# Performance work log

Hardware: AMD Instinct MI355X
Metric: run time of the kernel (lower is better)

The kernel has to match this reference:

```python
import jax, jax.numpy as jnp
import numpy as np
import math

SUB_LEN = 5

def _row_mask(index, sub_len, win_len):
    # Faithful port of logsparseAttention.row_mask (numpy, built at trace time).
    log_l = math.ceil(math.log2(sub_len))
    mask = np.zeros(win_len, dtype=np.float32)
    if (win_len // sub_len) * 2 * log_l > index:
        mask[: index + 1] = 1.0
    else:
        while index >= 0:
            if index - log_l + 1 < 0:
                mask[:index] = 1.0
                break
            mask[index - log_l + 1 : index + 1] = 1.0
            for i in range(log_l):
                new_index = index - log_l + 1 - 2 ** i
                if index - new_index <= sub_len and new_index >= 0:
                    mask[new_index] = 1.0
            index -= sub_len
    return mask

def _log_mask(win_len, sub_len):
    m = np.stack([_row_mask(i, sub_len, win_len) for i in range(win_len)])
    return m[None, None]  # [1, 1, L, L]

def setup_inputs() -> dict:
    key = jax.random.key(0)
    kq, kk, kv = jax.random.split(key, 3)
    B, L, H, D = 4, 2048, 16, 64
    return {
        "queries": jax.random.normal(kq, (B, L, H, D), dtype=jnp.float32),
        "keys": jax.random.normal(kk, (B, L, H, D), dtype=jnp.float32),
        "values": jax.random.normal(kv, (B, L, H, D), dtype=jnp.float32),
        "attn_mask": jnp.zeros((1,), dtype=jnp.int32),  # unused by the module
    }

def reference(queries, keys, values, attn_mask):
    L = queries.shape[1]
    mask = jnp.asarray(_log_mask(L, SUB_LEN), dtype=queries.dtype)  # [1,1,L,L]
    q = jnp.swapaxes(queries, 1, 2)            # [B, H, L, D]
    k = jnp.transpose(keys, (0, 2, 3, 1))      # [B, H, D, L]
    v = jnp.swapaxes(values, 1, 2)             # [B, H, L, D]
    pre_att = jnp.matmul(q, k)                 # [B, H, L, L] (no scaling: scale=None)
    pre_att = pre_att * mask + (-1e9) * (1.0 - mask)
    att = jax.nn.softmax(pre_att, axis=-1)
    return jnp.matmul(att, v)                  # [B, H, L, D]
```

## Files before the change

kernel.cpp:

```cpp
#include <hip/hip_runtime.h>


typedef __attribute__((ext_vector_type(8))) short short8;
typedef __attribute__((ext_vector_type(4))) float floatx4;
typedef _Float16 half8 __attribute__((ext_vector_type(8)));
typedef _Float16 half4 __attribute__((ext_vector_type(4)));

#define NB 4
#define NL 2048
#define NH 16
#define ND 64
#define PADK 72
#define PADQ 72

static __device__ __forceinline__ unsigned short f2bf(float f) {
    unsigned int u = __float_as_uint(f);
    u += 0x7fff + ((u >> 16) & 1);
    return (unsigned short)(u >> 16);
}
static __device__ __forceinline__ float bf2f(unsigned short h) {
    return __uint_as_float(((unsigned int)h) << 16);
}

__global__ __launch_bounds__(256)
void conv_kv(const float* __restrict__ Kg, const float* __restrict__ Vg,
             _Float16* __restrict__ Kf, _Float16* __restrict__ Vt) {
    __shared__ float tile[64][65];
    const int kt = blockIdx.x;
    const int bh = blockIdx.y;
    const int b  = bh >> 4, h = bh & 15;
    const int t  = threadIdx.x;
    const int row = t >> 2;
    const int seg = (t & 3) * 16;
    const size_t gsrc = (((size_t)(b * NL + kt * 64 + row) * NH + h) << 6) + seg;
    {
        float kv[16];
        #pragma unroll
        for (int i = 0; i < 16; i += 4) *(float4*)(kv + i) = *(const float4*)(Kg + gsrc + i);
        half8 o0, o1;
        #pragma unroll
        for (int j2 = 0; j2 < 8; ++j2) { o0[j2] = (_Float16)kv[j2]; o1[j2] = (_Float16)kv[8 + j2]; }
        _Float16* kd = Kf + (((size_t)(bh * NL + kt * 64 + row)) << 6) + seg;
        *(half8*)kd = o0;
        *(half8*)(kd + 8) = o1;
    }
    {
        #pragma unroll
        for (int i = 0; i < 16; i += 4) {
            float4 v = *(const float4*)(Vg + gsrc + i);
            tile[row][seg + i + 0] = v.x;
            tile[row][seg + i + 1] = v.y;
            tile[row][seg + i + 2] = v.z;
            tile[row][seg + i + 3] = v.w;
        }
    }
    __syncthreads();
    #pragma unroll
    for (int pass = 0; pass < 2; ++pass) {
        const int d  = pass * 32 + (t >> 3);
        const int kk = (t & 7) * 8;
        half8 o;
        #pragma unroll
        for (int j2 = 0; j2 < 8; ++j2) o[j2] = (_Float16)tile[kk + j2][d];
        *(half8*)(Vt + (((size_t)(bh * 64 + d)) << 11) + kt * 64 + kk) = o;
    }
}

__global__ __launch_bounds__(256, 2)
void lsattn_main(const float* __restrict__ Qg,
                 const _Float16* __restrict__ Kf,
                 const _Float16* __restrict__ Vt,
                 float* __restrict__ Og) {
    __shared__ alignas(16) _Float16 Ks[64 * PADK];
    __shared__ alignas(16) _Float16 Vs[64 * PADK];
    __shared__ alignas(16) _Float16 Ps[4 * 16 * PADQ];

    const int id   = (int)blockIdx.x;
    const int bh   = id & 63;
    const int pr   = id >> 6;
    const int tid  = threadIdx.x;
    const int lane = tid & 63;
    const int w    = tid >> 6;
    const int col  = lane & 15;
    const int quad = lane >> 4;

    const int base128 = (w < 2) ? pr : (15 - pr);
    const int qbase   = base128 * 128 + (w & 1) * 64;
    const int sa      = qbase >> 6;

    half8 qf[4][2];
    #pragma unroll
    for (int qc = 0; qc < 4; ++qc) {
        const float* qp = Qg + (((size_t)((bh >> 4) * NL + qbase + qc * 16 + col) * NH + (bh & 15)) << 6) + quad * 8;
        #pragma unroll
        for (int c = 0; c < 2; ++c) {
            float4 a = *(const float4*)(qp + c * 32);
            float4 b = *(const float4*)(qp + c * 32 + 4);
            qf[qc][c][0] = (_Float16)a.x; qf[qc][c][1] = (_Float16)a.y;
            qf[qc][c][2] = (_Float16)a.z; qf[qc][c][3] = (_Float16)a.w;
            qf[qc][c][4] = (_Float16)b.x; qf[qc][c][5] = (_Float16)b.y;
            qf[qc][c][6] = (_Float16)b.z; qf[qc][c][7] = (_Float16)b.w;
        }
    }

    floatx4 ofrag[4][4];
    #pragma unroll
    for (int qc = 0; qc < 4; ++qc)
        #pragma unroll
        for (int mc = 0; mc < 4; ++mc) ofrag[qc][mc] = floatx4{0.f, 0.f, 0.f, 0.f};
    float m_run[4] = {-1e30f, -1e30f, -1e30f, -1e30f};
    float l_run[4] = {0.f, 0.f, 0.f, 0.f};

    const int srow = tid >> 2;
    const int sseg = (tid & 3) * 16;
    const _Float16* kgb = Kf + (((size_t)(bh * NL)) << 6) + (srow << 6) + sseg;
    const _Float16* vgb = Vt + (((size_t)bh) << 17) + ((size_t)srow << 11) + sseg;
    _Float16* pbuf = Ps + w * 16 * PADQ;

    const int TB = 31 - 2 * pr;

    half8 kpre0 = *(const half8*)(kgb);
    half8 kpre1 = *(const half8*)(kgb + 8);
    half8 vpre0 = *(const half8*)(vgb);
    half8 vpre1 = *(const half8*)(vgb + 8);

    for (int t = 0; t <= TB; ++t) {
        const int j0 = t * 64;
        __syncthreads();
        *(half8*)(Ks + srow * PADK + sseg)     = kpre0;
        *(half8*)(Ks + srow * PADK + sseg + 8) = kpre1;
        *(half8*)(Vs + srow * PADK + sseg)     = vpre0;
        *(half8*)(Vs + srow * PADK + sseg + 8) = vpre1;
        if (t < TB) {
            kpre0 = *(const half8*)(kgb + (t + 1) * 4096);
            kpre1 = *(const half8*)(kgb + (t + 1) * 4096 + 8);
            vpre0 = *(const half8*)(vgb + (t + 1) * 64);
            vpre1 = *(const half8*)(vgb + (t + 1) * 64 + 8);
        }
        __syncthreads();

        if (t > sa) continue;

        half8 kfr[4][2], vfr[4][2];
        #pragma unroll
        for (int f = 0; f < 4; ++f) {
            kfr[f][0] = *(const half8*)(Ks + (f * 16 + col) * PADK + quad * 8);
            kfr[f][1] = *(const half8*)(Ks + (f * 16 + col) * PADK + 32 + quad * 8);
            vfr[f][0] = *(const half8*)(Vs + (f * 16 + col) * PADK + quad * 8);
            vfr[f][1] = *(const half8*)(Vs + (f * 16 + col) * PADK + 32 + quad * 8);
        }

        const bool diag = (t == sa);
        #pragma unroll
        for (int qc = 0; qc < 4; ++qc) {
            const int qrow = qbase + qc * 16 + col;

            floatx4 stf[4];
            #pragma unroll
            for (int f = 0; f < 4; ++f) {
                floatx4 acc = floatx4{0.f, 0.f, 0.f, 0.f};
                acc = __builtin_amdgcn_mfma_f32_16x16x32_f16(kfr[f][0], qf[qc][0], acc, 0, 0, 0);
                acc = __builtin_amdgcn_mfma_f32_16x16x32_f16(kfr[f][1], qf[qc][1], acc, 0, 0, 0);
                stf[f] = acc;
            }

            if (diag) {
                #pragma unroll
                for (int f = 0; f < 4; ++f)
                    #pragma unroll
                    for (int r = 0; r < 4; ++r) {
                        const int key = j0 + f * 16 + quad * 4 + r;
                        if (key > qrow) stf[f][r] = -1e30f;
                    }
            }

            float mt = -1e30f;
            #pragma unroll
            for (int f = 0; f < 4; ++f)
                #pragma unroll
                for (int r = 0; r < 4; ++r) mt = fmaxf(mt, stf[f][r]);
            mt = fmaxf(mt, __shfl_xor(mt, 16));
            mt = fmaxf(mt, __shfl_xor(mt, 32));
            const float m_new = fmaxf(m_run[qc], mt);
            const float alpha = __expf(m_run[qc] - m_new);
            float ls = 0.f;
            #pragma unroll
            for (int f = 0; f < 4; ++f)
                #pragma unroll
                for (int r = 0; r < 4; ++r) {
                    const float p = __expf(stf[f][r] - m_new);
                    stf[f][r] = p;
                    ls += p;
                }
            ls += __shfl_xor(ls, 16);
            ls += __shfl_xor(ls, 32);
            l_run[qc] = l_run[qc] * alpha + ls;
            m_run[qc] = m_new;
            #pragma unroll
            for (int mc = 0; mc < 4; ++mc) ofrag[qc][mc] *= alpha;

            #pragma unroll
            for (int f = 0; f < 4; ++f) {
                half4 hp;
                hp[0] = (_Float16)stf[f][0]; hp[1] = (_Float16)stf[f][1];
                hp[2] = (_Float16)stf[f][2]; hp[3] = (_Float16)stf[f][3];
                *(half4*)(pbuf + col * PADQ + f * 16 + quad * 4) = hp;
            }
            half8 pf0 = *(const half8*)(pbuf + col * PADQ + quad * 8);
            half8 pf1 = *(const half8*)(pbuf + col * PADQ + 32 + quad * 8);

            #pragma unroll
            for (int mc = 0; mc < 4; ++mc) {
                ofrag[qc][mc] = __builtin_amdgcn_mfma_f32_16x16x32_f16(vfr[mc][0], pf0, ofrag[qc][mc], 0, 0, 0);
                ofrag[qc][mc] = __builtin_amdgcn_mfma_f32_16x16x32_f16(vfr[mc][1], pf1, ofrag[qc][mc], 0, 0, 0);
            }
        }
    }

    #pragma unroll
    for (int qc = 0; qc < 4; ++qc) {
        const float inv = 1.f / l_run[qc];
        float* op = Og + ((size_t)bh * NL + qbase + qc * 16 + col) * ND;
        #pragma unroll
        for (int mc = 0; mc < 4; ++mc) {
            float4 o;
            o.x = ofrag[qc][mc][0] * inv;
            o.y = ofrag[qc][mc][1] * inv;
            o.z = ofrag[qc][mc][2] * inv;
            o.w = ofrag[qc][mc][3] * inv;
            *(float4*)(op + mc * 16 + quad * 4) = o;
        }
    }
}

__global__ __launch_bounds__(256)
void lsattn_fb(const float* __restrict__ Qg,
               const float* __restrict__ Kg,
               const float* __restrict__ Vg,
               float* __restrict__ Og) {
    __shared__ alignas(16) unsigned short Kh[64 * PADK];
    __shared__ alignas(16) unsigned short Kl[64 * PADK];
    __shared__ alignas(16) unsigned short Vh[64 * PADK];

    const int qt   = 31 - (int)blockIdx.x;
    const int bh   = blockIdx.y;
    const int tid  = threadIdx.x;
    const int lane = tid & 63;
    const int w    = tid >> 6;
    const int col  = lane & 15;
    const int quad = lane >> 4;
    const int qrow = qt * 64 + w * 16 + col;

    short8 qhi[2], qlo[2];
    {
        const float* qp = Qg + ((bh >> 4) * NL + qrow) * (NH * ND) + (bh & 15) * ND + quad * 8;
        #pragma unroll
        for (int c = 0; c < 2; ++c) {
            float qv[8];
            *(float4*)(qv + 0) = *(const float4*)(qp + c * 32);
            *(float4*)(qv + 4) = *(const float4*)(qp + c * 32 + 4);
            #pragma unroll
            for (int j = 0; j < 8; ++j) {
                unsigned short h = f2bf(qv[j]);
                qhi[c][j] = (short)h;
                qlo[c][j] = (short)f2bf(qv[j] - bf2f(h));
            }
        }
    }
    floatx4 ofrag[4];
    #pragma unroll
    for (int i = 0; i < 4; ++i) ofrag[i] = floatx4{0.f, 0.f, 0.f, 0.f};
    float m_run = -1e30f, l_run = 0.f;
    const int skey  = tid >> 2;
    const int sdb   = (tid & 3) * 16;
    const int gbase = (bh >> 4) * NL * NH * ND + (bh & 15) * ND;

    for (int t = 0; t <= qt; ++t) {
        const int j0 = t * 64;
        __syncthreads();
        {
            const int gro = gbase + (j0 + skey) * (NH * ND) + sdb;
            float kv[16], vv[16];
            #pragma unroll
            for (int i = 0; i < 16; i += 4) {
                *(float4*)(kv + i) = *(const float4*)(Kg + gro + i);
                *(float4*)(vv + i) = *(const float4*)(Vg + gro + i);
            }
            short8 h0, h1, l0, l1;
            #pragma unroll
            for (int j = 0; j < 8; ++j) {
                unsigned short h = f2bf(kv[j]);
                h0[j] = (short)h; l0[j] = (short)f2bf(kv[j] - bf2f(h));
                unsigned short g = f2bf(kv[8 + j]);
                h1[j] = (short)g; l1[j] = (short)f2bf(kv[8 + j] - bf2f(g));
            }
            *(short8*)(Kh + skey * PADK + sdb)     = h0;
            *(short8*)(Kh + skey * PADK + sdb + 8) = h1;
            *(short8*)(Kl + skey * PADK + sdb)     = l0;
            *(short8*)(Kl + skey * PADK + sdb + 8) = l1;
            #pragma unroll
            for (int i = 0; i < 16; ++i) Vh[(sdb + i) * PADK + skey] = f2bf(vv[i]);
        }
        __syncthreads();

        floatx4 stf[4];
        #pragma unroll
        for (int f = 0; f < 4; ++f) {
            floatx4 acc = floatx4{0.f, 0.f, 0.f, 0.f};
            #pragma unroll
            for (int c = 0; c < 2; ++c) {
                short8 kh = *(const short8*)(Kh + (f * 16 + col) * PADK + c * 32 + quad * 8);
                short8 kl = *(const short8*)(Kl + (f * 16 + col) * PADK + c * 32 + quad * 8);
                acc = __builtin_amdgcn_mfma_f32_16x16x32_bf16(kh, qhi[c], acc, 0, 0, 0);
                acc = __builtin_amdgcn_mfma_f32_16x16x32_bf16(kl, qhi[c], acc, 0, 0, 0);
                acc = __builtin_amdgcn_mfma_f32_16x16x32_bf16(kh, qlo[c], acc, 0, 0, 0);
            }
            stf[f] = acc;
        }
        if (t == qt) {
            #pragma unroll
            for (int f = 0; f < 4; ++f)
                #pragma unroll
                for (int r = 0; r < 4; ++r) {
                    const int key = j0 + f * 16 + quad * 4 + r;
                    if (key > qrow) stf[f][r] = -1e30f;
                }
        }
        float mt = -1e30f;
        #pragma unroll
        for (int f = 0; f < 4; ++f)
            #pragma unroll
            for (int r = 0; r < 4; ++r) mt = fmaxf(mt, stf[f][r]);
        mt = fmaxf(mt, __shfl_xor(mt, 16));
        mt = fmaxf(mt, __shfl_xor(mt, 32));
        const float m_new = fmaxf(m_run, mt);
        const float alpha = __expf(m_run - m_new);
        float ls = 0.f;
        #pragma unroll
        for (int f = 0; f < 4; ++f)
            #pragma unroll
            for (int r = 0; r < 4; ++r) {
                const float p = __expf(stf[f][r] - m_new);
                stf[f][r] = p; ls += p;
            }
        ls += __shfl_xor(ls, 16);
        ls += __shfl_xor(ls, 32);
        l_run = l_run * alpha + ls;
        m_run = m_new;
        #pragma unroll
        for (int mc = 0; mc < 4; ++mc) ofrag[mc] *= alpha;

        short8 pfrag[2];
        #pragma unroll
        for (int kc = 0; kc < 2; ++kc) {
            #pragma unroll
            for (int jj = 0; jj < 8; ++jj) {
                const int r  = jj & 3;
                const int sq = (quad & 1) * 2 + (jj >> 2);
                const int sl = col + (sq << 4);
                const float va = __shfl(stf[kc * 2 + 0][r], sl);
                const float vb = __shfl(stf[kc * 2 + 1][r], sl);
                pfrag[kc][jj] = (short)f2bf((quad & 2) ? vb : va);
            }
        }
        #pragma unroll
        for (int mc = 0; mc < 4; ++mc) {
            #pragma unroll
            for (int kc = 0; kc < 2; ++kc) {
                short8 vf = *(const short8*)(Vh + (mc * 16 + col) * PADK + kc * 32 + quad * 8);
                ofrag[mc] = __builtin_amdgcn_mfma_f32_16x16x32_bf16(vf, pfrag[kc], ofrag[mc], 0, 0, 0);
            }
        }
    }
    const float inv = 1.f / l_run;
    float* op = Og + ((size_t)bh * NL + qrow) * ND;
    #pragma unroll
    for (int mc = 0; mc < 4; ++mc) {
        float4 o;
        o.x = ofrag[mc][0] * inv; o.y = ofrag[mc][1] * inv;
        o.z = ofrag[mc][2] * inv; o.w = ofrag[mc][3] * inv;
        *(float4*)(op + mc * 16 + quad * 4) = o;
    }
}

extern "C" void kernel_launch(void* const* d_in, const int* in_sizes, int n_in,
                              void* d_out, int out_size, void* d_ws, size_t ws_size,
                              hipStream_t stream) {
    const float* Q = (const float*)d_in[0];
    const float* K = (const float*)d_in[1];
    const float* V = (const float*)d_in[2];
    float* O = (float*)d_out;

    const size_t elems = (size_t)NB * NL * NH * ND;
    if (ws_size >= 2 * elems * sizeof(_Float16)) {
        _Float16* Kf = (_Float16*)d_ws;
        _Float16* Vt = Kf + elems;
        conv_kv<<<dim3(32, 64), dim3(256), 0, stream>>>(K, V, Kf, Vt);
        lsattn_main<<<dim3(512), dim3(256), 0, stream>>>(Q, Kf, Vt, O);
    } else {
        lsattn_fb<<<dim3(32, 64), dim3(256), 0, stream>>>(Q, K, V, O);
    }
}
```

Before: 215.7 us.

## Halve per-block query tile to 64 rows, double grid, raise occupancy

Each block now covers two 64-row query segments (a paired front/back causal split) instead of two 128-row segments. Each wave handles 32 query rows in two interleaved 16-row chunks. K and V fragments are read from LDS right before use instead of being held in registers. The smaller register footprint allows launch bounds of 4 blocks per CU, and the grid is doubled to 1024 blocks to improve latency hiding and load balance. In exchange, each K/V tile staged into LDS is reused by fewer query rows, so global and LDS traffic per unit of compute goes up.

```diff
diff --git a/kernel.cpp b/kernel.cpp
--- a/kernel.cpp
+++ b/kernel.cpp
@@ -66,14 +66,14 @@
     }
 }
 
-__global__ __launch_bounds__(256, 2)
+__global__ __launch_bounds__(256, 4)
 void lsattn_main(const float* __restrict__ Qg,
                  const _Float16* __restrict__ Kf,
                  const _Float16* __restrict__ Vt,
                  float* __restrict__ Og) {
     __shared__ alignas(16) _Float16 Ks[64 * PADK];
     __shared__ alignas(16) _Float16 Vs[64 * PADK];
-    __shared__ alignas(16) _Float16 Ps[4 * 16 * PADQ];
+    __shared__ alignas(16) _Float16 Ps[8 * 16 * PADQ];
 
     const int id   = (int)blockIdx.x;
     const int bh   = id & 63;
@@ -84,13 +84,13 @@
     const int col  = lane & 15;
     const int quad = lane >> 4;
 
-    const int base128 = (w < 2) ? pr : (15 - pr);
-    const int qbase   = base128 * 128 + (w & 1) * 64;
-    const int sa      = qbase >> 6;
-
-    half8 qf[4][2];
-    #pragma unroll
-    for (int qc = 0; qc < 4; ++qc) {
+    const int s64   = (w < 2) ? pr : (31 - pr);
+    const int qbase = s64 * 64 + (w & 1) * 32;
+    const int sa    = s64;
+
+    half8 qf[2][2];
+    #pragma unroll
+    for (int qc = 0; qc < 2; ++qc) {
         const float* qp = Qg + (((size_t)((bh >> 4) * NL + qbase + qc * 16 + col) * NH + (bh & 15)) << 6) + quad * 8;
         #pragma unroll
         for (int c = 0; c < 2; ++c) {
@@ -103,21 +103,22 @@
         }
     }
 
-    floatx4 ofrag[4][4];
-    #pragma unroll
-    for (int qc = 0; qc < 4; ++qc)
+    floatx4 ofrag[2][4];
+    #pragma unroll
+    for (int qc = 0; qc < 2; ++qc)
         #pragma unroll
         for (int mc = 0; mc < 4; ++mc) ofrag[qc][mc] = floatx4{0.f, 0.f, 0.f, 0.f};
-    float m_run[4] = {-1e30f, -1e30f, -1e30f, -1e30f};
-    float l_run[4] = {0.f, 0.f, 0.f, 0.f};
+    float m_run[2] = {-1e30f, -1e30f};
+    float l_run[2] = {0.f, 0.f};
 
     const int srow = tid >> 2;
     const int sseg = (tid & 3) * 16;
     const _Float16* kgb = Kf + (((size_t)(bh * NL)) << 6) + (srow << 6) + sseg;
     const _Float16* vgb = Vt + (((size_t)bh) << 17) + ((size_t)srow << 11) + sseg;
-    _Float16* pbuf = Ps + w * 16 * PADQ;
-
-    const int TB = 31 - 2 * pr;
+    _Float16* pbuf0 = Ps + (w * 2 + 0) * 16 * PADQ;
+    _Float16* pbuf1 = Ps + (w * 2 + 1) * 16 * PADQ;
+
+    const int TB = 31 - pr;
 
     half8 kpre0 = *(const half8*)(kgb);
     half8 kpre1 = *(const half8*)(kgb + 8);
@@ -141,84 +142,97 @@
 
         if (t > sa) continue;
 
-        half8 kfr[4][2], vfr[4][2];
-        #pragma unroll
-        for (int f = 0; f < 4; ++f) {
-            kfr[f][0] = *(const half8*)(Ks + (f * 16 + col) * PADK + quad * 8);
-            kfr[f][1] = *(const half8*)(Ks + (f * 16 + col) * PADK + 32 + quad * 8);
-            vfr[f][0] = *(const half8*)(Vs + (f * 16 + col) * PADK + quad * 8);
-            vfr[f][1] = *(const half8*)(Vs + (f * 16 + col) * PADK + 32 + quad * 8);
-        }
-
-        const bool diag = (t == sa);
-        #pragma unroll
-        for (int qc = 0; qc < 4; ++qc) {
-            const int qrow = qbase + qc * 16 + col;
-
-            floatx4 stf[4];
+        floatx4 stf0[4], stf1[4];
+        {
             #pragma unroll
             for (int f = 0; f < 4; ++f) {
-                floatx4 acc = floatx4{0.f, 0.f, 0.f, 0.f};
-                acc = __builtin_amdgcn_mfma_f32_16x16x32_f16(kfr[f][0], qf[qc][0], acc, 0, 0, 0);
-                acc = __builtin_amdgcn_mfma_f32_16x16x32_f16(kfr[f][1], qf[qc][1], acc, 0, 0, 0);
-                stf[f] = acc;
-            }
-
-            if (diag) {
-                #pragma unroll
-                for (int f = 0; f < 4; ++f)
-                    #pragma unroll
-                    for (int r = 0; r < 4; ++r) {
-                        const int key = j0 + f * 16 + quad * 4 + r;
-                        if (key > qrow) stf[f][r] = -1e30f;
-                    }
-            }
-
-            float mt = -1e30f;
-            #pragma unroll
-            for (int f = 0; f < 4; ++f)
-                #pragma unroll
-                for (int r = 0; r < 4; ++r) mt = fmaxf(mt, stf[f][r]);
-            mt = fmaxf(mt, __shfl_xor(mt, 16));
-            mt = fmaxf(mt, __shfl_xor(mt, 32));
-            const float m_new = fmaxf(m_run[qc], mt);
-            const float alpha = __expf(m_run[qc] - m_new);
-            float ls = 0.f;
+                half8 k0 = *(const half8*)(Ks + (f * 16 + col) * PADK + quad * 8);
+                half8 k1 = *(const half8*)(Ks + (f * 16 + col) * PADK + 32 + quad * 8);
+                floatx4 a0 = floatx4{0.f, 0.f, 0.f, 0.f};
+                a0 = __builtin_amdgcn_mfma_f32_16x16x32_f16(k0, qf[0][0], a0, 0, 0, 0);
+                a0 = __builtin_amdgcn_mfma_f32_16x16x32_f16(k1, qf[0][1], a0, 0, 0, 0);
+                stf0[f] = a0;
+                floatx4 a1 = floatx4{0.f, 0.f, 0.f, 0.f};
+                a1 = __builtin_amdgcn_mfma_f32_16x16x32_f16(k0, qf[1][0], a1, 0, 0, 0);
+                a1 = __builtin_amdgcn_mfma_f32_16x16x32_f16(k1, qf[1][1], a1, 0, 0, 0);
+                stf1[f] = a1;
+            }
+        }
+
+        if (t == sa) {
             #pragma unroll
             for (int f = 0; f < 4; ++f)
                 #pragma unroll
                 for (int r = 0; r < 4; ++r) {
-                    const float p = __expf(stf[f][r] - m_new);
-                    stf[f][r] = p;
-                    ls += p;
+                    const int key = j0 + f * 16 + quad * 4 + r;
+                    if (key > qbase + col)      stf0[f][r] = -1e30f;
+                    if (key > qbase + 16 + col) stf1[f][r] = -1e30f;
                 }
-            ls += __shfl_xor(ls, 16);
-            ls += __shfl_xor(ls, 32);
-            l_run[qc] = l_run[qc] * alpha + ls;
-            m_run[qc] = m_new;
-            #pragma unroll
-            for (int mc = 0; mc < 4; ++mc) ofrag[qc][mc] *= alpha;
-
-            #pragma unroll
-            for (int f = 0; f < 4; ++f) {
-                half4 hp;
-                hp[0] = (_Float16)stf[f][0]; hp[1] = (_Float16)stf[f][1];
-                hp[2] = (_Float16)stf[f][2]; hp[3] = (_Float16)stf[f][3];
-                *(half4*)(pbuf + col * PADQ + f * 16 + quad * 4) = hp;
-            }
-            half8 pf0 = *(const half8*)(pbuf + col * PADQ + quad * 8);
-            half8 pf1 = *(const half8*)(pbuf + col * PADQ + 32 + quad * 8);
-
-            #pragma unroll
-            for (int mc = 0; mc < 4; ++mc) {
-                ofrag[qc][mc] = __builtin_amdgcn_mfma_f32_16x16x32_f16(vfr[mc][0], pf0, ofrag[qc][mc], 0, 0, 0);
-                ofrag[qc][mc] = __builtin_amdgcn_mfma_f32_16x16x32_f16(vfr[mc][1], pf1, ofrag[qc][mc], 0, 0, 0);
-            }
-        }
-    }
-
-    #pragma unroll
-    for (int qc = 0; qc < 4; ++qc) {
+        }
+
+        float mt0 = -1e30f, mt1 = -1e30f;
+        #pragma unroll
+        for (int f = 0; f < 4; ++f)
+            #pragma unroll
+            for (int r = 0; r < 4; ++r) {
+                mt0 = fmaxf(mt0, stf0[f][r]);
+                mt1 = fmaxf(mt1, stf1[f][r]);
+            }
+        mt0 = fmaxf(mt0, __shfl_xor(mt0, 16));
+        mt1 = fmaxf(mt1, __shfl_xor(mt1, 16));
+        mt0 = fmaxf(mt0, __shfl_xor(mt0, 32));
+        mt1 = fmaxf(mt1, __shfl_xor(mt1, 32));
+        const float mn0 = fmaxf(m_run[0], mt0);
+        const float mn1 = fmaxf(m_run[1], mt1);
+        const float al0 = __expf(m_run[0] - mn0);
+        const float al1 = __expf(m_run[1] - mn1);
+        float ls0 = 0.f, ls1 = 0.f;
+        #pragma unroll
+        for (int f = 0; f < 4; ++f)
+            #pragma unroll
+            for (int r = 0; r < 4; ++r) {
+                const float p0 = __expf(stf0[f][r] - mn0);
+                const float p1 = __expf(stf1[f][r] - mn1);
+                stf0[f][r] = p0; ls0 += p0;
+                stf1[f][r] = p1; ls1 += p1;
+            }
+        ls0 += __shfl_xor(ls0, 16);
+        ls1 += __shfl_xor(ls1, 16);
+        ls0 += __shfl_xor(ls0, 32);
+        ls1 += __shfl_xor(ls1, 32);
+        l_run[0] = l_run[0] * al0 + ls0;  m_run[0] = mn0;
+        l_run[1] = l_run[1] * al1 + ls1;  m_run[1] = mn1;
+        #pragma unroll
+        for (int mc = 0; mc < 4; ++mc) { ofrag[0][mc] *= al0; ofrag[1][mc] *= al1; }
+
+        #pragma unroll
+        for (int f = 0; f < 4; ++f) {
+            half4 h0, h1;
+            h0[0] = (_Float16)stf0[f][0]; h0[1] = (_Float16)stf0[f][1];
+            h0[2] = (_Float16)stf0[f][2]; h0[3] = (_Float16)stf0[f][3];
+            h1[0] = (_Float16)stf1[f][0]; h1[1] = (_Float16)stf1[f][1];
+            h1[2] = (_Float16)stf1[f][2]; h1[3] = (_Float16)stf1[f][3];
+            *(half4*)(pbuf0 + col * PADQ + f * 16 + quad * 4) = h0;
+            *(half4*)(pbuf1 + col * PADQ + f * 16 + quad * 4) = h1;
+        }
+        half8 pf00 = *(const half8*)(pbuf0 + col * PADQ + quad * 8);
+        half8 pf01 = *(const half8*)(pbuf0 + col * PADQ + 32 + quad * 8);
+        half8 pf10 = *(const half8*)(pbuf1 + col * PADQ + quad * 8);
+        half8 pf11 = *(const half8*)(pbuf1 + col * PADQ + 32 + quad * 8);
+
+        #pragma unroll
+        for (int mc = 0; mc < 4; ++mc) {
+            half8 v0 = *(const half8*)(Vs + (mc * 16 + col) * PADK + quad * 8);
+            half8 v1 = *(const half8*)(Vs + (mc * 16 + col) * PADK + 32 + quad * 8);
+            ofrag[0][mc] = __builtin_amdgcn_mfma_f32_16x16x32_f16(v0, pf00, ofrag[0][mc], 0, 0, 0);
+            ofrag[0][mc] = __builtin_amdgcn_mfma_f32_16x16x32_f16(v1, pf01, ofrag[0][mc], 0, 0, 0);
+            ofrag[1][mc] = __builtin_amdgcn_mfma_f32_16x16x32_f16(v0, pf10, ofrag[1][mc], 0, 0, 0);
+            ofrag[1][mc] = __builtin_amdgcn_mfma_f32_16x16x32_f16(v1, pf11, ofrag[1][mc], 0, 0, 0);
+        }
+    }
+
+    #pragma unroll
+    for (int qc = 0; qc < 2; ++qc) {
         const float inv = 1.f / l_run[qc];
         float* op = Og + ((size_t)bh * NL + qbase + qc * 16 + col) * ND;
         #pragma unroll
@@ -396,7 +410,7 @@
         _Float16* Kf = (_Float16*)d_ws;
         _Float16* Vt = Kf + elems;
         conv_kv<<<dim3(32, 64), dim3(256), 0, stream>>>(K, V, Kf, Vt);
-        lsattn_main<<<dim3(512), dim3(256), 0, stream>>>(Q, Kf, Vt, O);
+        lsattn_main<<<dim3(1024), dim3(256), 0, stream>>>(Q, Kf, Vt, O);
     } else {
         lsattn_fb<<<dim3(32, 64), dim3(256), 0, stream>>>(Q, K, V, O);
     }
```

New measurement: 200.6 us. -7.0%, faster.
